# Kernel tuning notes

Hardware: AMD Instinct MI355X
Metric: run time of the kernel (lower is better)

Reference implementation:

```python
import jax, jax.numpy as jnp
import numpy as np

T, B, E, H = 2048, 2, 2048, 16
D = E // H  # 128


def setup_inputs() -> dict:
    key = jax.random.key(0)
    ks = jax.random.split(key, 4)
    query = jax.random.normal(ks[0], (T, B, E), dtype=jnp.float32)
    Wqkv = jax.random.normal(ks[1], (3 * E, E), dtype=jnp.float32) * 0.02
    bqkv = jnp.zeros((3 * E,), dtype=jnp.float32)
    Wo = jax.random.normal(ks[2], (E, E), dtype=jnp.float32) * 0.02
    bo = jnp.zeros((E,), dtype=jnp.float32)
    # Llama rotary frequencies: freqs_cis[t, j] = exp(i * t * theta^{-2j/D})
    inv_freq = 1.0 / (10000.0 ** (np.arange(0, D, 2, dtype=np.float32) / D))  # (D/2,)
    angles = np.arange(T, dtype=np.float32)[:, None] * inv_freq[None, :]       # (T, D/2)
    freqs_cos = jnp.asarray(np.cos(angles), dtype=jnp.float32)
    freqs_sin = jnp.asarray(np.sin(angles), dtype=jnp.float32)
    return {"query": query, "Wqkv": Wqkv, "bqkv": bqkv, "Wo": Wo, "bo": bo,
            "freqs_cos": freqs_cos, "freqs_sin": freqs_sin}


def _apply_rope(x, cos, sin):
    # Faithful to metaseq: x is (T, B, E) but view()-ed as (B, T, H, D);
    # jnp.reshape is the same row-major reinterpretation as torch .view().
    xr = x.reshape(B, T, H, D // 2, 2)
    x0, x1 = xr[..., 0], xr[..., 1]
    c = cos[None, :, None, :]  # broadcast over batch and heads, seq_dim=1
    s = sin[None, :, None, :]
    o0 = x0 * c - x1 * s
    o1 = x0 * s + x1 * c
    return jnp.stack([o0, o1], axis=-1).reshape(T, B, E)


def reference(query, Wqkv, bqkv, Wo, bo, freqs_cos, freqs_sin):
    # Combined QKV projection (ColumnParallelLinear, world_size=1), split order (k, v, q)
    kvq = jnp.einsum('tbe,fe->tbf', query, Wqkv) + bqkv  # (T, B, 3E)
    k, v, q = jnp.split(kvq, 3, axis=-1)
    q = _apply_rope(q, freqs_cos, freqs_sin)
    k = _apply_rope(k, freqs_cos, freqs_sin)
    # scaling split as sqrt(head_dim^-0.5) on both q and k (baddbmm path)
    s = jnp.asarray(D, jnp.float32) ** -0.25
    qb = q.reshape(T, B * H, D).swapaxes(0, 1) * s   # (BH, T, D)
    kb = k.reshape(T, B * H, D).swapaxes(0, 1) * s   # (BH, S, D)
    vb = v.reshape(T, B * H, D).swapaxes(0, 1)       # (BH, S, D)
    scores = jnp.einsum('btd,bsd->bts', qb, kb)      # (BH, T, S)
    causal = jnp.tril(jnp.ones((T, T), dtype=bool))  # ScaledUpperTriangMaskedSoftmax
    scores = jnp.where(causal[None, :, :], scores, jnp.finfo(scores.dtype).min)
    probs = jax.nn.softmax(scores, axis=-1)          # dropout p=0 -> identity
    attn = jnp.einsum('bts,bsd->btd', probs, vb)     # (BH, T, D)
    attn = attn.swapaxes(0, 1).reshape(T, B, E)
    # RowParallelLinear with skip_bias_add=True: bias returned separately (not added)
    out = jnp.einsum('tbe,fe->tbf', attn, Wo)
    return out
```

## Files before the change

kernel.cpp:

```cpp
#include <hip/hip_runtime.h>
#include <stdint.h>

typedef unsigned short u16;
typedef __attribute__((ext_vector_type(4))) float f32x4;
typedef __attribute__((ext_vector_type(8))) short bf16x8;
typedef __attribute__((ext_vector_type(8))) u16 u16x8;

#define T_SEQ  2048
#define EMB    2048
#define HD     128
#define NHEAD  16
#define NTOK   4096
#define NE3    6144
#define SCALE  0.29730177875068026f
#define LOG2E  1.44269504088896f

typedef __attribute__((address_space(3))) char* lds_t;
typedef const __attribute__((address_space(1))) char* gl_t;

__device__ __forceinline__ void gld16(const void* g, void* l) {
  __builtin_amdgcn_global_load_lds((gl_t)g, (lds_t)l, 16, 0, 0);
}

__device__ __forceinline__ u16 f2bf(float f) {
  union { float f; uint32_t u; } c; c.f = f;
  uint32_t r = c.u + 0x7fffu + ((c.u >> 16) & 1u);
  return (u16)(r >> 16);
}

__global__ __launch_bounds__(256) void cvt_bf16(const float* __restrict__ in,
                                                u16* __restrict__ out, int n8) {
  int i = blockIdx.x * 256 + threadIdx.x;
  if (i >= n8) return;
  const float4* p = (const float4*)in + (size_t)i * 2;
  float4 a = p[0], b = p[1];
  u16x8 o;
  o[0]=f2bf(a.x); o[1]=f2bf(a.y); o[2]=f2bf(a.z); o[3]=f2bf(a.w);
  o[4]=f2bf(b.x); o[5]=f2bf(b.y); o[6]=f2bf(b.z); o[7]=f2bf(b.w);
  *((u16x8*)out + i) = o;
}


__device__ __forceinline__ bf16x8 rdfrag(const char* slot, int row, int lq) {
  return *(const bf16x8*)(slot + row*64 + ((lq ^ ((row >> 1) & 3)) << 4));
}
__device__ __forceinline__ void stageA(const char* Ag, int K2, int ktb, int ks,
                                       char* slot, int tid) {
  int row = tid >> 2, c = tid & 3;
  gld16(Ag + (size_t)row*K2 + ktb + ks*64 + ((c ^ ((row >> 1) & 3)) << 4),
        slot + tid*16);
}
__device__ __forceinline__ void stageB(const char* Bg, int K2, int ktb, int ks,
                                       char* slot, int j, int tid) {
  int lb = j*8192 + tid*16;
  int row = lb >> 6, c = (lb >> 4) & 3;
  gld16(Bg + (size_t)row*K2 + ktb + ks*64 + ((c ^ ((row >> 1) & 3)) << 4),
        slot + lb);
}

template<int EPI, int NBN>
__global__ __launch_bounds__(512, 2) void gemmP(
    const u16* __restrict__ A, const u16* __restrict__ Bm, int K, int N,
    const float* __restrict__ cosT, const float* __restrict__ sinT,
    const float* __restrict__ bias,
    u16* __restrict__ Qh, u16* __restrict__ Kh, u16* __restrict__ Vt,
    float* __restrict__ Cout)
{
  __shared__ __align__(16) char lds[98304];
  const int tid = threadIdx.x;
  const int lane = tid & 63, w = tid >> 6;
  const int wm = w >> 2, wn = w & 3;
  const int l15 = lane & 15, lq = lane >> 4;

  const int q8 = gridDim.x >> 3;
  const int swz = (blockIdx.x & 7) * q8 + (blockIdx.x >> 3);
  const int bM = swz / NBN, bN = swz % NBN;

  const char* Ag = (const char*)(A + (size_t)bM * 128 * K);
  const char* Bg = (const char*)(Bm + (size_t)bN * 256 * K);
  const int K2 = K * 2;
  const int nT = K >> 6;

  stageA(Ag, K2, 0,   0, lds + 0,     tid);
  stageB(Bg, K2, 0,   0, lds + 32768, 0, tid);
  stageB(Bg, K2, 0,   0, lds + 32768, 1, tid);
  stageA(Ag, K2, 0,   1, lds + 8192,  tid);
  stageB(Bg, K2, 0,   1, lds + 49152, 0, tid);
  stageB(Bg, K2, 0,   1, lds + 49152, 1, tid);
  stageA(Ag, K2, 128, 0, lds + 16384, tid);
  stageB(Bg, K2, 128, 0, lds + 65536, 0, tid);
  stageB(Bg, K2, 128, 0, lds + 65536, 1, tid);

  f32x4 acc[4][4] = {};

  for (int t = 0; t < nT; ++t) {
    #pragma unroll
    for (int ks = 0; ks < 2; ++ks) {
      const int q = 2*t + ks;
      const int ts = (q + 3) >> 1, kss = (q + 3) & 1;
      const int tsc = ts < nT ? ts : nT - 1;
      const char* Asl = lds + ((t & 1)*2 + ks)*8192;
      const char* Bsl = lds + 32768 + ((t & 1)*2 + ks)*16384;
      char* AslS = lds + ((ts & 1)*2 + kss)*8192;
      char* BslS = lds + 32768 + ((ts & 1)*2 + kss)*16384;

      asm volatile("s_waitcnt vmcnt(6)" ::: "memory");
      __builtin_amdgcn_s_barrier();
      __builtin_amdgcn_sched_barrier(0);

      bf16x8 af[4], bf[4];
      #pragma unroll
      for (int i = 0; i < 4; i++) af[i] = rdfrag(Asl, wm*64 + i*16 + l15, lq);
      #pragma unroll
      for (int i = 0; i < 4; i++) bf[i] = rdfrag(Bsl, wn*64 + i*16 + l15, lq);
      stageA(Ag, K2, tsc << 7, kss, AslS, tid);
      stageB(Bg, K2, tsc << 7, kss, BslS, 0, tid);
      stageB(Bg, K2, tsc << 7, kss, BslS, 1, tid);
      asm volatile("s_waitcnt lgkmcnt(0)" ::: "memory");
      __builtin_amdgcn_sched_barrier(0);
      __builtin_amdgcn_s_setprio(1);
      #pragma unroll
      for (int mi = 0; mi < 4; mi++)
        #pragma unroll
        for (int ni = 0; ni < 4; ni++)
          acc[mi][ni] = __builtin_amdgcn_mfma_f32_16x16x32_bf16(af[mi], bf[ni], acc[mi][ni], 0, 0, 0);
      __builtin_amdgcn_s_setprio(0);
    }
  }
  asm volatile("s_waitcnt vmcnt(0)" ::: "memory");

  if (EPI == 0) {
    #pragma unroll
    for (int mi = 0; mi < 4; mi++) {
      int row = bM*128 + wm*64 + mi*16 + lq*4;
      #pragma unroll
      for (int ni = 0; ni < 4; ni++) {
        int col = bN*256 + wn*64 + ni*16 + l15;
        #pragma unroll
        for (int r = 0; r < 4; r++)
          Cout[(size_t)(row + r) * N + col] = acc[mi][ni][r];
      }
    }
  } else {
    const int cbase = bN*256 + wn*64;
    const int seg  = cbase >> 11;
    const int head = (cbase >> 7) & 15;
    #pragma unroll
    for (int mi = 0; mi < 4; mi++) {
      #pragma unroll
      for (int ni = 0; ni < 4; ni++) {
        int col = cbase + ni*16 + l15;
        int d = col & 127;
        float bi = bias[col];
        f32x4 v = acc[mi][ni];
        #pragma unroll
        for (int r = 0; r < 4; r++) {
          int n = bM*128 + wm*64 + mi*16 + lq*4 + r;
          float val = v[r] + bi;
          int t = n >> 1, b = n & 1;
          int bh = b*NHEAD + head;
          if (seg == 1) {
            Vt[((size_t)bh*HD + d)*T_SEQ + t] = f2bf(val);
          } else {
            float par = __shfl_xor(val, 1);
            int fidx = d >> 1;
            float cs = cosT[(n & (T_SEQ-1))*64 + fidx];
            float sn = sinT[(n & (T_SEQ-1))*64 + fidx];
            val = (d & 1) ? (par*sn + val*cs) : (val*cs - par*sn);
            val *= SCALE;
            u16* dst = (seg == 0) ? Kh : Qh;
            dst[((size_t)bh*T_SEQ + t)*HD + d] = f2bf(val);
          }
        }
      }
    }
  }
}

__global__ __launch_bounds__(256, 4) void attn_fwd(
    const u16* __restrict__ Qh, const u16* __restrict__ Kh,
    const u16* __restrict__ Vt, u16* __restrict__ O)
{
  const int i = blockIdx.x;
  const int kk = i >> 8, c = i & 255;
  const int bh = (c >> 5) + kk * 8;
  const int b5 = c & 31;
  const int qb = (kk & 1) ? (31 - b5) : b5;

  const int tid = threadIdx.x, lane = tid & 63, w = tid >> 6;
  const int l15 = lane & 15, lq = lane >> 4;

  __shared__ u16 Ks[64*128];
  __shared__ u16 Vs[128*64];
  __shared__ char Ps[4][2048];

  const int q0 = qb*64 + w*16;
  bf16x8 qf[4];
  #pragma unroll
  for (int dc = 0; dc < 4; dc++)
    qf[dc] = *(const bf16x8*)(Qh + ((size_t)bh*T_SEQ + q0 + l15)*HD + dc*32 + lq*8);

  f32x4 o[8] = {};
  float m[4], l_[4];
  #pragma unroll
  for (int r = 0; r < 4; r++) { m[r] = -1e30f; l_[r] = 0.f; }

  const int nkb = qb + 1;
  for (int kb = 0; kb < nkb; ++kb) {
    #pragma unroll
    for (int j = 0; j < 4; j++) {
      int lb = tid*16 + j*4096;
      int row = lb >> 8, bir = lb & 255;
      int sb = bir ^ ((row & 7) << 4);
      gld16((const char*)Kh + (((size_t)bh*T_SEQ + kb*64 + row) << 8) + sb,
            (char*)Ks + lb);
    }
    #pragma unroll
    for (int j = 0; j < 4; j++) {
      int lb = tid*16 + j*4096;
      int row = lb >> 7, bir = lb & 127;
      int sb = bir ^ ((row & 7) << 4);
      gld16((const char*)Vt + ((size_t)(bh*HD + row)*T_SEQ)*2 + kb*128 + sb,
            (char*)Vs + lb);
    }
    __syncthreads();

    f32x4 sacc[4];
    #pragma unroll
    for (int nf = 0; nf < 4; nf++) {
      f32x4 z = {};
      sacc[nf] = z;
      #pragma unroll
      for (int dc = 0; dc < 4; dc++) {
        int row = nf*16 + l15;
        int bir = (dc*64 + lq*16) ^ ((row & 7) << 4);
        bf16x8 kf = *(const bf16x8*)((const char*)Ks + row*256 + bir);
        sacc[nf] = __builtin_amdgcn_mfma_f32_16x16x32_bf16(qf[dc], kf, sacc[nf], 0, 0, 0);
      }
    }

    if (kb == qb) {
      #pragma unroll
      for (int nf = 0; nf < 4; nf++)
        #pragma unroll
        for (int r = 0; r < 4; r++) {
          int key = kb*64 + nf*16 + l15;
          int qr  = q0 + lq*4 + r;
          if (key > qr) sacc[nf][r] = -1e30f;
        }
    }

    #pragma unroll
    for (int r = 0; r < 4; r++) {
      float mx = fmaxf(fmaxf(sacc[0][r], sacc[1][r]), fmaxf(sacc[2][r], sacc[3][r]));
      mx = fmaxf(mx, __shfl_xor(mx, 1));
      mx = fmaxf(mx, __shfl_xor(mx, 2));
      mx = fmaxf(mx, __shfl_xor(mx, 4));
      mx = fmaxf(mx, __shfl_xor(mx, 8));
      float newm = fmaxf(m[r], mx);
      float scale = exp2f((m[r] - newm) * LOG2E);
      float sum = 0.f;
      #pragma unroll
      for (int nf = 0; nf < 4; nf++) {
        float p = exp2f((sacc[nf][r] - newm) * LOG2E);
        sacc[nf][r] = p;
        sum += p;
      }
      sum += __shfl_xor(sum, 1);
      sum += __shfl_xor(sum, 2);
      sum += __shfl_xor(sum, 4);
      sum += __shfl_xor(sum, 8);
      l_[r] = l_[r] * scale + sum;
      m[r] = newm;
      #pragma unroll
      for (int nf = 0; nf < 8; nf++) o[nf][r] *= scale;
    }

    #pragma unroll
    for (int nf = 0; nf < 4; nf++)
      #pragma unroll
      for (int r = 0; r < 4; r++) {
        int prow = lq*4 + r;
        int pbyte = prow*128 + ((((nf*16 + l15)*2)) ^ ((prow & 7) << 4));
        *(u16*)(Ps[w] + pbyte) = f2bf(sacc[nf][r]);
      }

    #pragma unroll
    for (int kc = 0; kc < 2; kc++) {
      int pb = (kc*64 + lq*16) ^ ((l15 & 7) << 4);
      bf16x8 pf = *(const bf16x8*)(Ps[w] + l15*128 + pb);
      #pragma unroll
      for (int nf = 0; nf < 8; nf++) {
        int row = nf*16 + l15;
        int bir = (kc*64 + lq*16) ^ ((row & 7) << 4);
        bf16x8 vf = *(const bf16x8*)((const char*)Vs + row*128 + bir);
        o[nf] = __builtin_amdgcn_mfma_f32_16x16x32_bf16(pf, vf, o[nf], 0, 0, 0);
      }
    }
    __syncthreads();
  }

  const int b = bh >> 4, h = bh & 15;
  #pragma unroll
  for (int r = 0; r < 4; r++) {
    float inv = 1.0f / l_[r];
    int t = q0 + lq*4 + r;
    size_t base = ((size_t)(t*2 + b))*EMB + h*HD;
    #pragma unroll
    for (int nf = 0; nf < 8; nf++)
      O[base + nf*16 + l15] = f2bf(o[nf][r] * inv);
  }
}

extern "C" void kernel_launch(void* const* d_in, const int* in_sizes, int n_in,
                              void* d_out, int out_size, void* d_ws, size_t ws_size,
                              hipStream_t stream) {
  const float* query = (const float*)d_in[0];
  const float* Wqkv  = (const float*)d_in[1];
  const float* bqkv  = (const float*)d_in[2];
  const float* Wo    = (const float*)d_in[3];
  const float* fcos  = (const float*)d_in[5];
  const float* fsin  = (const float*)d_in[6];
  float* out = (float*)d_out;
  char* ws = (char*)d_ws;

  u16* WQb = (u16*)(ws + 0);
  u16* WOb = (u16*)(ws + 25165824);
  u16* A1  = (u16*)(ws + 33554432);
  u16* QH  = (u16*)(ws + 50331648);
  u16* KH  = (u16*)(ws + 67108864);
  u16* VT  = (u16*)(ws + 83886080);

  cvt_bf16<<<4096, 256, 0, stream>>>(query, A1, 1048576);
  cvt_bf16<<<6144, 256, 0, stream>>>(Wqkv, WQb, 1572864);
  cvt_bf16<<<2048, 256, 0, stream>>>(Wo,   WOb,  524288);

  gemmP<1, 24><<<768, 512, 0, stream>>>(A1, WQb, 2048, NE3,
                                        fcos, fsin, bqkv, QH, KH, VT, nullptr);

  attn_fwd<<<1024, 256, 0, stream>>>(QH, KH, VT, A1);

  gemmP<0, 8><<<256, 512, 0, stream>>>(A1, WOb, 2048, EMB,
                                       nullptr, nullptr, nullptr,
                                       nullptr, nullptr, nullptr, out);
}
```

Baseline: 350.0 us.

## Deepen GEMM LDS pipeline to six stages and remap blocks into L2 regions

The GEMM prefetch ring grows from 4 to 6 LDS slots with 5 k-steps in flight. The loop now walks per k-half with rotating read and write slot indices and a waitcnt of vmcnt(12), so more global-load latency can be hidden. Block indices are also remapped into 4x8-by-4 tile regions so neighbouring blocks share A and B rows in L2. The cost is 144KB of LDS per block, which probably drops residency from two blocks per CU to one. The new mapping is hardcoded to the grid shapes used here.

```diff
diff --git a/kernel.cpp b/kernel.cpp
--- a/kernel.cpp
+++ b/kernel.cpp
@@ -66,66 +66,69 @@
     u16* __restrict__ Qh, u16* __restrict__ Kh, u16* __restrict__ Vt,
     float* __restrict__ Cout)
 {
-  __shared__ __align__(16) char lds[98304];
+  __shared__ __align__(16) char lds[147456];
   const int tid = threadIdx.x;
   const int lane = tid & 63, w = tid >> 6;
   const int wm = w >> 2, wn = w & 3;
   const int l15 = lane & 15, lq = lane >> 4;
 
-  const int q8 = gridDim.x >> 3;
-  const int swz = (blockIdx.x & 7) * q8 + (blockIdx.x >> 3);
-  const int bM = swz / NBN, bN = swz % NBN;
+  const int i = blockIdx.x;
+  const int r = i >> 8, x = i & 7, s = (i >> 3) & 31;
+  const int regionId = r*8 + x;
+  const int RM = regionId & 3, RN = regionId >> 2;
+  const int bM = RM*8 + (s >> 2);
+  const int bN = RN*4 + (s & 3);
 
   const char* Ag = (const char*)(A + (size_t)bM * 128 * K);
   const char* Bg = (const char*)(Bm + (size_t)bN * 256 * K);
   const int K2 = K * 2;
   const int nT = K >> 6;
-
-  stageA(Ag, K2, 0,   0, lds + 0,     tid);
-  stageB(Bg, K2, 0,   0, lds + 32768, 0, tid);
-  stageB(Bg, K2, 0,   0, lds + 32768, 1, tid);
-  stageA(Ag, K2, 0,   1, lds + 8192,  tid);
-  stageB(Bg, K2, 0,   1, lds + 49152, 0, tid);
-  stageB(Bg, K2, 0,   1, lds + 49152, 1, tid);
-  stageA(Ag, K2, 128, 0, lds + 16384, tid);
-  stageB(Bg, K2, 128, 0, lds + 65536, 0, tid);
-  stageB(Bg, K2, 128, 0, lds + 65536, 1, tid);
+  const int nQ = 2*nT;
+
+  #pragma unroll
+  for (int q = 0; q < 5; ++q) {
+    int kt = (q >> 1) << 7, ks = q & 1;
+    stageA(Ag, K2, kt, ks, lds + q*8192, tid);
+    stageB(Bg, K2, kt, ks, lds + 49152 + q*16384, 0, tid);
+    stageB(Bg, K2, kt, ks, lds + 49152 + q*16384, 1, tid);
+  }
 
   f32x4 acc[4][4] = {};
-
-  for (int t = 0; t < nT; ++t) {
-    #pragma unroll
-    for (int ks = 0; ks < 2; ++ks) {
-      const int q = 2*t + ks;
-      const int ts = (q + 3) >> 1, kss = (q + 3) & 1;
-      const int tsc = ts < nT ? ts : nT - 1;
-      const char* Asl = lds + ((t & 1)*2 + ks)*8192;
-      const char* Bsl = lds + 32768 + ((t & 1)*2 + ks)*16384;
-      char* AslS = lds + ((ts & 1)*2 + kss)*8192;
-      char* BslS = lds + 32768 + ((ts & 1)*2 + kss)*16384;
-
-      asm volatile("s_waitcnt vmcnt(6)" ::: "memory");
-      __builtin_amdgcn_s_barrier();
-      __builtin_amdgcn_sched_barrier(0);
-
-      bf16x8 af[4], bf[4];
-      #pragma unroll
-      for (int i = 0; i < 4; i++) af[i] = rdfrag(Asl, wm*64 + i*16 + l15, lq);
-      #pragma unroll
-      for (int i = 0; i < 4; i++) bf[i] = rdfrag(Bsl, wn*64 + i*16 + l15, lq);
-      stageA(Ag, K2, tsc << 7, kss, AslS, tid);
-      stageB(Bg, K2, tsc << 7, kss, BslS, 0, tid);
-      stageB(Bg, K2, tsc << 7, kss, BslS, 1, tid);
-      asm volatile("s_waitcnt lgkmcnt(0)" ::: "memory");
-      __builtin_amdgcn_sched_barrier(0);
-      __builtin_amdgcn_s_setprio(1);
-      #pragma unroll
-      for (int mi = 0; mi < 4; mi++)
-        #pragma unroll
-        for (int ni = 0; ni < 4; ni++)
-          acc[mi][ni] = __builtin_amdgcn_mfma_f32_16x16x32_bf16(af[mi], bf[ni], acc[mi][ni], 0, 0, 0);
-      __builtin_amdgcn_s_setprio(0);
-    }
+  int sRd = 0, sWr = 5;
+
+  for (int q = 0; q < nQ; ++q) {
+    const int qs = q + 5;
+    const int tsc = (qs >> 1) < nT ? (qs >> 1) : nT - 1;
+    const int kss = qs & 1;
+    const char* Asl = lds + sRd*8192;
+    const char* Bsl = lds + 49152 + sRd*16384;
+    char* AslS = lds + sWr*8192;
+    char* BslS = lds + 49152 + sWr*16384;
+
+    asm volatile("s_waitcnt vmcnt(12)" ::: "memory");
+    __builtin_amdgcn_s_barrier();
+    __builtin_amdgcn_sched_barrier(0);
+
+    bf16x8 af[4], bf[4];
+    #pragma unroll
+    for (int j = 0; j < 4; j++) af[j] = rdfrag(Asl, wm*64 + j*16 + l15, lq);
+    #pragma unroll
+    for (int j = 0; j < 4; j++) bf[j] = rdfrag(Bsl, wn*64 + j*16 + l15, lq);
+    stageA(Ag, K2, tsc << 7, kss, AslS, tid);
+    stageB(Bg, K2, tsc << 7, kss, BslS, 0, tid);
+    stageB(Bg, K2, tsc << 7, kss, BslS, 1, tid);
+    asm volatile("s_waitcnt lgkmcnt(0)" ::: "memory");
+    __builtin_amdgcn_sched_barrier(0);
+    __builtin_amdgcn_s_setprio(1);
+    #pragma unroll
+    for (int mi = 0; mi < 4; mi++)
+      #pragma unroll
+      for (int ni = 0; ni < 4; ni++)
+        acc[mi][ni] = __builtin_amdgcn_mfma_f32_16x16x32_bf16(af[mi], bf[ni], acc[mi][ni], 0, 0, 0);
+    __builtin_amdgcn_s_setprio(0);
+
+    sRd = sRd + 1 < 6 ? sRd + 1 : 0;
+    sWr = sWr + 1 < 6 ? sWr + 1 : 0;
   }
   asm volatile("s_waitcnt vmcnt(0)" ::: "memory");
 
@@ -137,8 +140,8 @@
       for (int ni = 0; ni < 4; ni++) {
         int col = bN*256 + wn*64 + ni*16 + l15;
         #pragma unroll
-        for (int r = 0; r < 4; r++)
-          Cout[(size_t)(row + r) * N + col] = acc[mi][ni][r];
+        for (int rr = 0; rr < 4; rr++)
+          Cout[(size_t)(row + rr) * N + col] = acc[mi][ni][rr];
       }
     }
   } else {
@@ -154,9 +157,9 @@
         float bi = bias[col];
         f32x4 v = acc[mi][ni];
         #pragma unroll
-        for (int r = 0; r < 4; r++) {
-          int n = bM*128 + wm*64 + mi*16 + lq*4 + r;
-          float val = v[r] + bi;
+        for (int rr = 0; rr < 4; rr++) {
+          int n = bM*128 + wm*64 + mi*16 + lq*4 + rr;
+          float val = v[rr] + bi;
           int t = n >> 1, b = n & 1;
           int bh = b*NHEAD + head;
           if (seg == 1) {
```

Measured after the change: 340.9 us. -2.6%, faster.
